# Performance work log

Hardware: AMD Instinct MI355X
Metric: run time of the kernel (lower is better)

The kernel has to match this reference:

```python
import jax, jax.numpy as jnp
import numpy as np
import math

EMB = 64
NEG_INF = -1e30

def _layernorm(x, g, b, eps=1e-5):
    mu = jnp.mean(x, axis=-1, keepdims=True)
    var = jnp.mean((x - mu) ** 2, axis=-1, keepdims=True)
    return (x - mu) * jax.lax.rsqrt(var + eps) * g + b

def setup_inputs() -> dict:
    key = jax.random.key(0)
    ks = jax.random.split(key, 8)
    b, t, n, d = 16, 12, 307, EMB
    s = 1.0 / math.sqrt(d)
    inp = {
        'x': jax.random.normal(ks[0], (b, t, n, d), dtype=jnp.float32),
        'stg': jax.random.uniform(ks[1], (b, n, t, n), dtype=jnp.float32),
        'topk': 3,
        'q_w': jax.random.normal(ks[2], (d, d), dtype=jnp.float32) * s,
        'q_b': jnp.zeros((d,), jnp.float32),
        'k_w': jax.random.normal(ks[3], (d, d), dtype=jnp.float32) * s,
        'k_b': jnp.zeros((d,), jnp.float32),
        'ln_g': jnp.ones((d,), jnp.float32),
        'ln_b': jnp.zeros((d,), jnp.float32),
        'ffn_ln_g': jnp.ones((d,), jnp.float32),
        'ffn_ln_b': jnp.zeros((d,), jnp.float32),
        'fc1_w': jax.random.normal(ks[4], (4 * d, d), dtype=jnp.float32) * s,
        'fc1_b': jnp.zeros((4 * d,), jnp.float32),
        'fc2_w': jax.random.normal(ks[5], (d, 4 * d), dtype=jnp.float32) * (0.5 * s),
        'fc2_b': jnp.zeros((d,), jnp.float32),
    }
    return inp

def reference(x, stg, topk, q_w, q_b, k_w, k_b, ln_g, ln_b, ffn_ln_g, ffn_ln_b, fc1_w, fc1_b, fc2_w, fc2_b):
    b, t, n, d = x.shape
    scale = 1.0 / math.sqrt(d)
    x_ = _layernorm(x, ln_g, ln_b)           # [b,t,n,d]
    y_ = x_[:, -1]                            # [b,n,d] last timestep
    q = y_ @ q_w.T + q_b                      # [b,n,d]
    k = x_ @ k_w.T + k_b                      # [b,t,n,d]
    dg = jnp.einsum('bnd,btmd->bntm', q, k) * scale
    sag = jax.nn.sigmoid(dg) * stg * scale    # gated scores [b,n,t,n]
    sag = sag.reshape(b, n, t * n)
    if topk > 0:
        kk = topk * n if topk < 5 else topk   # mirrors torch's self.topk *= n
        top_values, _ = jax.lax.top_k(sag, kk)
        thr = top_values[..., -1:]
        sag = jnp.where(sag > thr, sag, NEG_INF)  # strict >, as in torch code
    sag = jax.nn.softmax(sag, axis=-1).reshape(b, n, t, n)  # dropout in eval mode = identity
    o = jnp.einsum('bntm,btmd->bnd', sag, x_)
    h = o + y_
    # FFN: pre-norm residual MLP (LayerNorm -> Linear(d,4d) -> ReLU -> Linear(4d,d) + residual)
    z = _layernorm(h, ffn_ln_g, ffn_ln_b)
    z = jax.nn.relu(z @ fc1_w.T + fc1_b) @ fc2_w.T + fc2_b
    return h + z
```

## Files before the change

### kernel.cpp

```cpp
#include <hip/hip_runtime.h>

typedef __bf16 bf16x8 __attribute__((ext_vector_type(8)));
typedef float  f32x4  __attribute__((ext_vector_type(4)));
typedef unsigned short u16x8 __attribute__((ext_vector_type(8)));

constexpr int BB    = 16;
constexpr int TT    = 12;
constexpr int NN    = 307;
constexpr int TN    = TT * NN;
constexpr int ROWSX = BB * TT * NN;
constexpr int ROWSH = BB * NN;
constexpr int SST1  = 3712;
constexpr int SSTR  = 3840;
constexpr float SCALE = 0.125f;

__device__ __forceinline__ float wred_sum(float v) {
#pragma unroll
    for (int m = 32; m > 0; m >>= 1) v += __shfl_xor(v, m, 64);
    return v;
}

__global__ void fold_k(const float* __restrict__ qw, const float* __restrict__ qb,
                       const float* __restrict__ kw, const float* __restrict__ kb,
                       float* __restrict__ M, float* __restrict__ b2,
                       float* __restrict__ vv, float* __restrict__ cc) {
    int e = blockIdx.x, d = threadIdx.x;
    float acc = 0.f;
    for (int dp = 0; dp < 64; ++dp) acc += qw[dp * 64 + e] * kw[dp * 64 + d];
    M[e * 64 + d] = acc;
    float vp = wred_sum(qw[d * 64 + e] * kb[d]);
    if (d == 0) vv[e] = vp;
    if (e == 0) {
        float b = 0.f;
        for (int dp = 0; dp < 64; ++dp) b += qb[dp] * kw[dp * 64 + d];
        b2[d] = b;
        float cp = wred_sum(qb[d] * kb[d]);
        if (d == 0) *cc = cp;
    }
}

__global__ void wconv_k(const float* __restrict__ fc1w, const float* __restrict__ fc2w,
                        __bf16* __restrict__ fc1b16, __bf16* __restrict__ fc2b16) {
    int i = blockIdx.x * 256 + threadIdx.x;
    if (i < 16384) fc1b16[i] = (__bf16)fc1w[i];
    else fc2b16[i - 16384] = (__bf16)fc2w[i - 16384];
}

__global__ __launch_bounds__(256) void ln_k(const float* __restrict__ x,
                                            const float* __restrict__ g,
                                            const float* __restrict__ b,
                                            __bf16* __restrict__ xnb,
                                            float* __restrict__ y32) {
    int w = threadIdx.x >> 6, l = threadIdx.x & 63;
    int r = blockIdx.x * 4 + w;
    if (r >= ROWSX) return;
    float val = x[r * 64 + l];
    float mu  = wred_sum(val) * (1.f / 64.f);
    float dv  = val - mu;
    float var = wred_sum(dv * dv) * (1.f / 64.f);
    float xv  = dv * rsqrtf(var + 1e-5f) * g[l] + b[l];
    xnb[(size_t)r * 64 + l] = (__bf16)xv;
    int t = (r / NN) % TT;
    if (t == TT - 1) {
        int bbv = r / (NN * TT), n = r % NN;
        y32[(bbv * NN + n) * 64 + l] = xv;
    }
}

__global__ __launch_bounds__(256) void t_k(const __bf16* __restrict__ xnb,
                                           __bf16* __restrict__ xnT) {
    __shared__ unsigned short tile[64][65];
    int bb = blockIdx.y, j0 = blockIdx.x * 64, t = threadIdx.x;
    const unsigned short* src = (const unsigned short*)xnb;
    unsigned short* dst = (unsigned short*)xnT;
#pragma unroll
    for (int i = 0; i < 16; ++i) {
        int f = t + 256 * i, jr = f >> 6, dc = f & 63;
        int j = j0 + jr;
        tile[jr][dc] = (j < TN) ? src[((size_t)bb * TN + j) * 64 + dc] : (unsigned short)0;
    }
    __syncthreads();
#pragma unroll
    for (int i = 0; i < 16; ++i) {
        int f = t + 256 * i, d = f >> 6, jj = f & 63;
        dst[((size_t)bb * 64 + d) * SSTR + j0 + jj] = tile[jj][d];
    }
}

__global__ __launch_bounds__(256) void qt_k(const float* __restrict__ y32,
                                            const float* __restrict__ M,
                                            const float* __restrict__ b2,
                                            const float* __restrict__ vv,
                                            const float* __restrict__ ccp,
                                            __bf16* __restrict__ qtb,
                                            float* __restrict__ cq) {
    int w = threadIdx.x >> 6, l = threadIdx.x & 63;
    int rr = blockIdx.x * 4 + w;
    if (rr >= ROWSH) return;
    float y = y32[rr * 64 + l];
    float acc = b2[l];
#pragma unroll
    for (int e = 0; e < 64; ++e) acc += __shfl(y, e, 64) * M[e * 64 + l];
    qtb[(size_t)rr * 64 + l] = (__bf16)acc;
    float cp = wred_sum(y * vv[l]);
    if (l == 0) cq[rr] = cp + *ccp;
}

__global__ __launch_bounds__(256) void score_k(const __bf16* __restrict__ qtb,
                                               const float* __restrict__ cq,
                                               const __bf16* __restrict__ xnb,
                                               const float* __restrict__ stg,
                                               __bf16* __restrict__ sag) {
    __shared__ float sstg[64 * 132];
    int bb = blockIdx.z, n0 = blockIdx.y * 64, j0 = blockIdx.x * 128;
    int t = threadIdx.x;
    int w = t >> 6, lane = t & 63;
    int m16 = lane & 15, q4 = lane >> 4;

#pragma unroll
    for (int i = 0; i < 8; ++i) {
        int flat = t + i * 256;
        int row = flat >> 5, c4 = (flat & 31) * 4;
        int n = n0 + row;
        float4 v = {0.f, 0.f, 0.f, 0.f};
        if (n < NN) {
            size_t rb = (size_t)(bb * NN + n) * TN;
            int j = j0 + c4;
            if (j + 3 < TN) v = *(const float4*)(stg + rb + j);
            else {
                if (j + 0 < TN) v.x = stg[rb + j + 0];
                if (j + 1 < TN) v.y = stg[rb + j + 1];
                if (j + 2 < TN) v.z = stg[rb + j + 2];
                if (j + 3 < TN) v.w = stg[rb + j + 3];
            }
        }
        *(float4*)&sstg[row * 132 + c4] = v;
    }

    const bf16x8* ap = (const bf16x8*)(qtb + ((size_t)bb * NN + n0 + w * 16 + m16) * 64);
    bf16x8 a0 = ap[q4], a1 = ap[q4 + 4];
    f32x4 acc[8];
#pragma unroll
    for (int jt = 0; jt < 8; ++jt) {
        const bf16x8* bp = (const bf16x8*)(xnb + ((size_t)bb * TN + j0 + jt * 16 + m16) * 64);
        bf16x8 b0 = bp[q4], b1 = bp[q4 + 4];
        f32x4 c = {0.f, 0.f, 0.f, 0.f};
        c = __builtin_amdgcn_mfma_f32_16x16x32_bf16(a0, b0, c, 0, 0, 0);
        c = __builtin_amdgcn_mfma_f32_16x16x32_bf16(a1, b1, c, 0, 0, 0);
        acc[jt] = c;
    }
    int nbase = n0 + w * 16 + q4 * 4;
    float cn[4];
#pragma unroll
    for (int r = 0; r < 4; ++r) {
        int n = nbase + r;
        cn[r] = (n < NN) ? cq[bb * NN + n] : 0.f;
    }
    __syncthreads();

    u16x8 wvr[4];
#pragma unroll
    for (int r = 0; r < 4; ++r) {
        int nloc = w * 16 + q4 * 4 + r;
#pragma unroll
        for (int jt = 0; jt < 8; ++jt) {
            int j = j0 + jt * 16 + m16;
            float sv = sstg[nloc * 132 + jt * 16 + m16];
            float dg = (acc[jt][r] + cn[r]) * SCALE;
            float s  = 1.f / (1.f + __expf(-dg));
            float wv = (j < TN) ? s * sv * SCALE : 0.f;
            __bf16 wb16 = (__bf16)wv;
            wvr[r][jt] = *(unsigned short*)&wb16;
        }
    }
    __syncthreads();

    unsigned short* wb = (unsigned short*)sstg;
#pragma unroll
    for (int r = 0; r < 4; ++r) {
        int nloc = w * 16 + q4 * 4 + r;
#pragma unroll
        for (int jt = 0; jt < 8; ++jt)
            wb[nloc * 136 + jt * 16 + m16] = wvr[r][jt];
    }
    __syncthreads();

#pragma unroll
    for (int i = 0; i < 4; ++i) {
        int chunk = t + i * 256;
        int row = chunk >> 4, c8 = (chunk & 15) * 8;
        int n = n0 + row;
        if (n < NN) {
            u16x8 v = *(const u16x8*)&wb[row * 136 + c8];
            *(u16x8*)((unsigned short*)sag + (size_t)(bb * NN + n) * SST1 + j0 + c8) = v;
        }
    }
}

__global__ __launch_bounds__(512) void attn_k(const __bf16* __restrict__ sagB,
                                              const __bf16* __restrict__ xnT,
                                              const float* __restrict__ y32,
                                              const int* __restrict__ topk_p,
                                              float* __restrict__ h) {
    __shared__ unsigned short sg[8][3720];
    __shared__ float red[4][8][16];
    int t = threadIdx.x;
    int bb = blockIdx.y, n0 = blockIdx.x * 8;
    int wid = t >> 6, lane = t & 63;
    int m16 = lane & 15, q4 = lane >> 4;

    int topkv = *topk_p;
    bool selAll = (topkv <= 0);
    int kk = 0;
    if (!selAll) {
        kk = (topkv < 5) ? topkv * NN : topkv;
        if (kk > TN) kk = TN;
    }

    int n = n0 + wid;
    const u16x8* src = (const u16x8*)((const unsigned short*)sagB +
                                      (size_t)(bb * NN + min(n, NN - 1)) * SST1);
    u16x8 va[8];
#pragma unroll
    for (int ci = 0; ci < 8; ++ci) {
        int c = lane + (ci << 6);
        u16x8 v = {0, 0, 0, 0, 0, 0, 0, 0};
        if (c < 464) v = src[c];
        va[ci] = v;
    }
    int vmb = 0;
#pragma unroll
    for (int ci = 0; ci < 8; ++ci)
#pragma unroll
        for (int e = 0; e < 8; ++e) vmb = max(vmb, (int)va[ci][e]);
#pragma unroll
    for (int m = 32; m > 0; m >>= 1) vmb = max(vmb, __shfl_xor(vmb, m, 64));
    float vmax = __uint_as_float(((unsigned)vmb) << 16);

    unsigned thrb = 0;
    if (!selAll) {
        unsigned lo = 0, hi = (unsigned)vmb;
        while (lo < hi) {
            unsigned mid = (lo + hi) >> 1;
            int cnt = 0;
#pragma unroll
            for (int ci = 0; ci < 8; ++ci)
#pragma unroll
                for (int e = 0; e < 8; ++e)
                    cnt += (int)__popcll(__ballot((unsigned)va[ci][e] > mid));
            if (cnt < kk) hi = mid; else lo = mid + 1;
        }
        thrb = lo;
    }

    float local = 0.f;
#pragma unroll
    for (int ci = 0; ci < 8; ++ci) {
        int c = lane + (ci << 6);
        int nvv = (c < 460) ? 8 : ((c == 460) ? 4 : 0);
#pragma unroll
        for (int e = 0; e < 8; ++e) {
            unsigned u = va[ci][e];
            bool sel = selAll ? (e < nvv) : (u > thrb);
            float ev = sel ? __expf(__uint_as_float(u << 16) - vmax) : 0.f;
            local += ev;
            __bf16 eb = (__bf16)ev;
            va[ci][e] = *(unsigned short*)&eb;
        }
    }
    local = wred_sum(local);
    bool uni = !(local > 0.f);
    float inv = uni ? 0.f : 1.f / local;
    float uval = 1.f / (float)TN;
#pragma unroll
    for (int ci = 0; ci < 8; ++ci) {
        int c = lane + (ci << 6);
        if (c < 464) {
            int nvv = (c < 460) ? 8 : ((c == 460) ? 4 : 0);
            bf16x8 o;
#pragma unroll
            for (int e = 0; e < 8; ++e) {
                if (uni) o[e] = (e < nvv) ? (__bf16)uval : (__bf16)0.f;
                else {
                    unsigned short us = va[ci][e];
                    float ev = (float)(*(__bf16*)&us);
                    o[e] = (__bf16)(ev * inv);
                }
            }
            *(bf16x8*)&sg[wid][c * 8] = o;
        }
    }
    __syncthreads();

    int dg = wid & 3, kh = wid >> 2;
    bf16x8 zf;
#pragma unroll
    for (int e = 0; e < 8; ++e) zf[e] = (__bf16)0.f;
    f32x4 acc0 = {0.f, 0.f, 0.f, 0.f}, acc1 = {0.f, 0.f, 0.f, 0.f};
    const __bf16* bbase = xnT + ((size_t)bb * 64 + dg * 16 + m16) * SSTR + q4 * 8;
    int kbeg = kh * 1856;
    for (int ks = 0; ks < 58; ks += 2) {
        int k0 = kbeg + ks * 32, k1 = k0 + 32;
        bf16x8 a0 = (m16 < 8) ? *(const bf16x8*)&sg[m16][k0 + q4 * 8] : zf;
        bf16x8 a1 = (m16 < 8) ? *(const bf16x8*)&sg[m16][k1 + q4 * 8] : zf;
        bf16x8 b0 = *(const bf16x8*)(bbase + k0);
        bf16x8 b1 = *(const bf16x8*)(bbase + k1);
        acc0 = __builtin_amdgcn_mfma_f32_16x16x32_bf16(a0, b0, acc0, 0, 0, 0);
        acc1 = __builtin_amdgcn_mfma_f32_16x16x32_bf16(a1, b1, acc1, 0, 0, 0);
    }
    if (kh == 0) {
        if (q4 < 2) {
#pragma unroll
            for (int r = 0; r < 4; ++r)
                red[dg][q4 * 4 + r][m16] = acc0[r] + acc1[r];
        }
    }
    __syncthreads();
    if (kh == 1 && q4 < 2) {
#pragma unroll
        for (int r = 0; r < 4; ++r) {
            int row = q4 * 4 + r;
            int nn2 = n0 + row;
            if (nn2 < NN) {
                size_t o = (size_t)(bb * NN + nn2) * 64 + dg * 16 + m16;
                h[o] = acc0[r] + acc1[r] + red[dg][row][m16] + y32[o];
            }
        }
    }
}

__global__ __launch_bounds__(256) void ffn_k(const float* __restrict__ h,
                                             const float* __restrict__ g,
                                             const float* __restrict__ bln,
                                             const __bf16* __restrict__ fc1b16,
                                             const float* __restrict__ fc1b,
                                             const __bf16* __restrict__ fc2b16,
                                             const float* __restrict__ fc2b,
                                             float* __restrict__ out) {
    __shared__ __bf16 zb[16 * 68];
    __shared__ __bf16 ab[16 * 264];
    int t = threadIdx.x, r0 = blockIdx.x * 16;
    int wid = t >> 6, lane = t & 63;
    int m16 = lane & 15, q4 = lane >> 4;

#pragma unroll
    for (int q = 0; q < 4; ++q) {
        int rl = wid * 4 + q;
        float val = h[(size_t)(r0 + rl) * 64 + lane];
        float mu  = wred_sum(val) * (1.f / 64.f);
        float dv  = val - mu;
        float var = wred_sum(dv * dv) * (1.f / 64.f);
        zb[rl * 68 + lane] = (__bf16)(dv * rsqrtf(var + 1e-5f) * g[lane] + bln[lane]);
    }
    __syncthreads();

    bf16x8 a0 = *(const bf16x8*)&zb[m16 * 68 + q4 * 8];
    bf16x8 a1 = *(const bf16x8*)&zb[m16 * 68 + 32 + q4 * 8];
#pragma unroll
    for (int jt2 = 0; jt2 < 4; ++jt2) {
        int j0t = (wid * 4 + jt2) * 16;
        const __bf16* bp = fc1b16 + (size_t)(j0t + m16) * 64 + q4 * 8;
        f32x4 c = {0.f, 0.f, 0.f, 0.f};
        c = __builtin_amdgcn_mfma_f32_16x16x32_bf16(a0, *(const bf16x8*)bp, c, 0, 0, 0);
        c = __builtin_amdgcn_mfma_f32_16x16x32_bf16(a1, *(const bf16x8*)(bp + 32), c, 0, 0, 0);
        int j = j0t + m16;
        float bias = fc1b[j];
#pragma unroll
        for (int r = 0; r < 4; ++r)
            ab[(q4 * 4 + r) * 264 + j] = (__bf16)fmaxf(c[r] + bias, 0.f);
    }
    __syncthreads();

    f32x4 c2a = {0.f, 0.f, 0.f, 0.f}, c2b = {0.f, 0.f, 0.f, 0.f};
    const __bf16* b2p = fc2b16 + (size_t)(wid * 16 + m16) * 256 + q4 * 8;
#pragma unroll
    for (int k8 = 0; k8 < 8; k8 += 2) {
        bf16x8 aa0 = *(const bf16x8*)&ab[m16 * 264 + k8 * 32 + q4 * 8];
        bf16x8 aa1 = *(const bf16x8*)&ab[m16 * 264 + (k8 + 1) * 32 + q4 * 8];
        c2a = __builtin_amdgcn_mfma_f32_16x16x32_bf16(aa0, *(const bf16x8*)(b2p + k8 * 32), c2a, 0, 0, 0);
        c2b = __builtin_amdgcn_mfma_f32_16x16x32_bf16(aa1, *(const bf16x8*)(b2p + (k8 + 1) * 32), c2b, 0, 0, 0);
    }
    int d = wid * 16 + m16;
    float bias2 = fc2b[d];
#pragma unroll
    for (int r = 0; r < 4; ++r) {
        size_t row = (size_t)(r0 + q4 * 4 + r);
        out[row * 64 + d] = h[row * 64 + d] + c2a[r] + c2b[r] + bias2;
    }
}

extern "C" void kernel_launch(void* const* d_in, const int* in_sizes, int n_in,
                              void* d_out, int out_size, void* d_ws, size_t ws_size,
                              hipStream_t stream) {
    const float* x    = (const float*)d_in[0];
    const float* stg  = (const float*)d_in[1];
    const int*   topk = (const int*)d_in[2];
    const float* qw   = (const float*)d_in[3];
    const float* qb   = (const float*)d_in[4];
    const float* kw   = (const float*)d_in[5];
    const float* kb   = (const float*)d_in[6];
    const float* lng  = (const float*)d_in[7];
    const float* lnb  = (const float*)d_in[8];
    const float* flng = (const float*)d_in[9];
    const float* flnb = (const float*)d_in[10];
    const float* fc1w = (const float*)d_in[11];
    const float* fc1b = (const float*)d_in[12];
    const float* fc2w = (const float*)d_in[13];
    const float* fc2b = (const float*)d_in[14];
    float* out = (float*)d_out;

    float* ws = (float*)d_ws;
    __bf16* xnb = (__bf16*)ws;
    float* p1   = ws + 1886208;
    __bf16* xnT = (__bf16*)p1;
    float* p2   = p1 + 1966080;
    __bf16* qtb = (__bf16*)p2;
    float* y32  = p2 + 157696;
    float* cq   = y32 + 314368;
    float* M    = cq + 4928;
    float* b2   = M + 4096;
    float* vv   = b2 + 64;
    float* cc   = vv + 64;
    __bf16* fc1b16 = (__bf16*)(cc + 16);
    __bf16* fc2b16 = (__bf16*)((float*)fc1b16 + 8192);
    __bf16* sag = (__bf16*)((float*)fc2b16 + 8192);
    float* h    = (float*)sag + 9116672;

    fold_k<<<64, 64, 0, stream>>>(qw, qb, kw, kb, M, b2, vv, cc);
    wconv_k<<<128, 256, 0, stream>>>(fc1w, fc2w, fc1b16, fc2b16);
    ln_k<<<(ROWSX + 3) / 4, 256, 0, stream>>>(x, lng, lnb, xnb, y32);
    t_k<<<dim3((TN + 63) / 64, BB), 256, 0, stream>>>(xnb, xnT);
    qt_k<<<(ROWSH + 3) / 4, 256, 0, stream>>>(y32, M, b2, vv, cc, qtb, cq);
    score_k<<<dim3((TN + 127) / 128, (NN + 63) / 64, BB), 256, 0, stream>>>(qtb, cq, xnb, stg, sag);
    attn_k<<<dim3((NN + 7) / 8, BB), 512, 0, stream>>>(sag, xnT, y32, topk, h);
    ffn_k<<<ROWSH / 16, 256, 0, stream>>>(h, flng, flnb, fc1b16, fc1b, fc2b16, fc2b, out);
}
```

Baseline: 274.5 us.

## Split attention into in-place top-k softmax kernel and separate MFMA PV kernel

After: 292.4 us. +6.5%, slower.

```diff
diff --git a/kernel.cpp b/kernel.cpp
--- a/kernel.cpp
+++ b/kernel.cpp
@@ -197,17 +197,12 @@
     }
 }
 
-__global__ __launch_bounds__(512) void attn_k(const __bf16* __restrict__ sagB,
-                                              const __bf16* __restrict__ xnT,
-                                              const float* __restrict__ y32,
-                                              const int* __restrict__ topk_p,
-                                              float* __restrict__ h) {
-    __shared__ unsigned short sg[8][3720];
-    __shared__ float red[4][8][16];
+__global__ __launch_bounds__(256) void smax_k(__bf16* __restrict__ sagB,
+                                              const int* __restrict__ topk_p) {
     int t = threadIdx.x;
-    int bb = blockIdx.y, n0 = blockIdx.x * 8;
     int wid = t >> 6, lane = t & 63;
-    int m16 = lane & 15, q4 = lane >> 4;
+    int row = blockIdx.x * 4 + wid;
+    if (row >= ROWSH) return;
 
     int topkv = *topk_p;
     bool selAll = (topkv <= 0);
@@ -217,9 +212,7 @@
         if (kk > TN) kk = TN;
     }
 
-    int n = n0 + wid;
-    const u16x8* src = (const u16x8*)((const unsigned short*)sagB +
-                                      (size_t)(bb * NN + min(n, NN - 1)) * SST1);
+    u16x8* src = (u16x8*)((unsigned short*)sagB + (size_t)row * SST1);
     u16x8 va[8];
 #pragma unroll
     for (int ci = 0; ci < 8; ++ci) {
@@ -287,44 +280,39 @@
                     o[e] = (__bf16)(ev * inv);
                 }
             }
-            *(bf16x8*)&sg[wid][c * 8] = o;
-        }
-    }
-    __syncthreads();
-
-    int dg = wid & 3, kh = wid >> 2;
-    bf16x8 zf;
-#pragma unroll
-    for (int e = 0; e < 8; ++e) zf[e] = (__bf16)0.f;
+            *(bf16x8*)&src[c] = o;
+        }
+    }
+}
+
+__global__ __launch_bounds__(256) void pv_k(const __bf16* __restrict__ sagB,
+                                            const __bf16* __restrict__ xnT,
+                                            const float* __restrict__ y32,
+                                            float* __restrict__ h) {
+    int bb = blockIdx.y, n0 = blockIdx.x * 16;
+    int wid = threadIdx.x >> 6, lane = threadIdx.x & 63;
+    int m16 = lane & 15, q4 = lane >> 4;
+
+    int arow = min(n0 + m16, NN - 1);
+    const __bf16* ab  = sagB + (size_t)(bb * NN + arow) * SST1 + q4 * 8;
+    const __bf16* bbp = xnT + ((size_t)bb * 64 + wid * 16 + m16) * SSTR + q4 * 8;
+
     f32x4 acc0 = {0.f, 0.f, 0.f, 0.f}, acc1 = {0.f, 0.f, 0.f, 0.f};
-    const __bf16* bbase = xnT + ((size_t)bb * 64 + dg * 16 + m16) * SSTR + q4 * 8;
-    int kbeg = kh * 1856;
-    for (int ks = 0; ks < 58; ks += 2) {
-        int k0 = kbeg + ks * 32, k1 = k0 + 32;
-        bf16x8 a0 = (m16 < 8) ? *(const bf16x8*)&sg[m16][k0 + q4 * 8] : zf;
-        bf16x8 a1 = (m16 < 8) ? *(const bf16x8*)&sg[m16][k1 + q4 * 8] : zf;
-        bf16x8 b0 = *(const bf16x8*)(bbase + k0);
-        bf16x8 b1 = *(const bf16x8*)(bbase + k1);
+#pragma unroll 4
+    for (int ks = 0; ks < 116; ks += 2) {
+        bf16x8 a0 = *(const bf16x8*)(ab + ks * 32);
+        bf16x8 b0 = *(const bf16x8*)(bbp + ks * 32);
+        bf16x8 a1 = *(const bf16x8*)(ab + ks * 32 + 32);
+        bf16x8 b1 = *(const bf16x8*)(bbp + ks * 32 + 32);
         acc0 = __builtin_amdgcn_mfma_f32_16x16x32_bf16(a0, b0, acc0, 0, 0, 0);
         acc1 = __builtin_amdgcn_mfma_f32_16x16x32_bf16(a1, b1, acc1, 0, 0, 0);
     }
-    if (kh == 0) {
-        if (q4 < 2) {
-#pragma unroll
-            for (int r = 0; r < 4; ++r)
-                red[dg][q4 * 4 + r][m16] = acc0[r] + acc1[r];
-        }
-    }
-    __syncthreads();
-    if (kh == 1 && q4 < 2) {
-#pragma unroll
-        for (int r = 0; r < 4; ++r) {
-            int row = q4 * 4 + r;
-            int nn2 = n0 + row;
-            if (nn2 < NN) {
-                size_t o = (size_t)(bb * NN + nn2) * 64 + dg * 16 + m16;
-                h[o] = acc0[r] + acc1[r] + red[dg][row][m16] + y32[o];
-            }
+#pragma unroll
+    for (int r = 0; r < 4; ++r) {
+        int n = n0 + q4 * 4 + r;
+        if (n < NN) {
+            size_t o = (size_t)(bb * NN + n) * 64 + wid * 16 + m16;
+            h[o] = acc0[r] + acc1[r] + y32[o];
         }
     }
 }
@@ -432,6 +420,7 @@
     t_k<<<dim3((TN + 63) / 64, BB), 256, 0, stream>>>(xnb, xnT);
     qt_k<<<(ROWSH + 3) / 4, 256, 0, stream>>>(y32, M, b2, vv, cc, qtb, cq);
     score_k<<<dim3((TN + 127) / 128, (NN + 63) / 64, BB), 256, 0, stream>>>(qtb, cq, xnb, stg, sag);
-    attn_k<<<dim3((NN + 7) / 8, BB), 512, 0, stream>>>(sag, xnT, y32, topk, h);
+    smax_k<<<(ROWSH + 3) / 4, 256, 0, stream>>>(sag, topk);
+    pv_k<<<dim3((NN + 15) / 16, BB), 256, 0, stream>>>(sag, xnT, y32, h);
     ffn_k<<<ROWSH / 16, 256, 0, stream>>>(h, flng, flnb, fc1b16, fc1b, fc2b16, fc2b, out);
 }
```
